# Performance work log

Hardware: AMD Instinct MI355X
Metric: run time of the kernel (lower is better)

Reference implementation:

```python
import jax, jax.numpy as jnp
import numpy as np

N_QUERIES = 32
N_KEYS = 128
INF = 1e10


def setup_inputs() -> dict:
    key = jax.random.key(0)
    kq, kk, kv = jax.random.split(key, 3)
    shape = (1, 16, 16384, 64)  # [B, H, N, d]
    return {
        "q": jax.random.normal(kq, shape, dtype=jnp.float32),
        "k": jax.random.normal(kk, shape, dtype=jnp.float32),
        "v": jax.random.normal(kv, shape, dtype=jnp.float32),
    }


def _local_attention(q, k, v, n_queries=N_QUERIES, n_keys=N_KEYS, inf=INF):
    # Faithful to torch _local_attention -> rearrange_to_dense_trunk -> _attention
    # (note: _attention applies NO 1/sqrt(d) scaling; we match that).
    n, d = q.shape[-2:]
    n_trunks = -(-n // n_queries)
    q_pad = n_trunks * n_queries - n
    pad_left = (n_keys - n_queries) // 2
    pad_right = int((n_trunks - 0.5) * n_queries + n_keys / 2 - n + 0.5)

    batch_dims = q.shape[:-2]
    # q -> [..., T, n_queries, d]
    qp = jnp.pad(q, [(0, 0)] * (q.ndim - 2) + [(0, q_pad), (0, 0)])
    q_t = qp.reshape(*batch_dims, n_trunks, n_queries, d)

    # k/v -> sliding windows [..., T, n_keys, d]; window t covers padded
    # positions [t*n_queries, t*n_queries + n_keys) (== torch unfold).
    win_idx = jnp.arange(n_trunks)[:, None] * n_queries + jnp.arange(n_keys)[None, :]

    def window(x):
        xp = jnp.pad(x, [(0, 0)] * (x.ndim - 2) + [(pad_left, pad_right), (0, 0)])
        return xp[..., win_idx, :]  # [..., T, n_keys, d]

    k_t = window(k)
    v_t = window(v)

    # Mask bias equivalent to the -inf padded attn_bias built in
    # rearrange_to_dense_trunk (attn_bias=None branch).
    t = jnp.arange(n_trunks)[:, None, None]
    qi = jnp.arange(n_queries)[None, :, None]
    kj = jnp.arange(n_keys)[None, None, :]
    key_pos = t * n_queries + kj - pad_left   # global key index
    row_pos = t * n_queries + qi              # global query index
    valid = (key_pos >= 0) & (key_pos < n) & (row_pos < n)
    bias = jnp.where(valid, jnp.zeros((), q.dtype), jnp.asarray(-inf, q.dtype))

    # blocked attention
    w = jnp.einsum('...tqd,...tkd->...tqk', q_t, k_t) + bias
    a = jax.nn.softmax(w, axis=-1)
    o = jnp.einsum('...tqk,...tkd->...tqd', a, v_t)

    o = o.reshape(*batch_dims, n_trunks * n_queries, d)
    return o[..., :n, :]


def reference(q, k, v):
    return _local_attention(q, k, v)
```

## Files before the change

kernel.cpp:

```cpp
#include <hip/hip_runtime.h>
#include <hip/hip_bf16.h>


typedef _Float16 f16x8 __attribute__((ext_vector_type(8)));
typedef _Float16 f16x4 __attribute__((ext_vector_type(4)));
typedef float f32x16 __attribute__((ext_vector_type(16)));
typedef unsigned int u32;
typedef u32 u32x4 __attribute__((ext_vector_type(4)));

#define NSEQ   16384
#define DHEAD  64
#define LOG2E  1.44269504088896340736f
#define TRB    4
#define BQ     (TRB * 32)
#define WROWS  (BQ + 96)
#define RSTR   128
#define KBYTES (WROWS * RSTR)

__device__ __forceinline__ int swz(int r) {
  return ((r & 7) << 4) | ((r & 8) << 3);
}

__device__ __forceinline__ u32 pk2(float a, float b) {
  auto h2 = __builtin_amdgcn_cvt_pkrtz(a, b);
  return __builtin_bit_cast(u32, h2);
}

__device__ __forceinline__ void plswap(u32& a, u32& b) {
#if __has_builtin(__builtin_amdgcn_permlane32_swap)
  typedef u32 u32x2 __attribute__((ext_vector_type(2)));
  u32x2 r = __builtin_amdgcn_permlane32_swap(a, b, false, false);
  a = r[0]; b = r[1];
#else
  const int hi = (threadIdx.x & 63) >> 5;
  u32 sa = (u32)__shfl_xor((int)a, 32);
  u32 sb = (u32)__shfl_xor((int)b, 32);
  u32 na = hi ? sb : a;
  u32 nb = hi ? b : sa;
  a = na; b = nb;
#endif
}

__device__ __forceinline__ void tr8(u32 va, f16x4 (&t)[8]) {
  asm volatile("ds_read_b64_tr_b16 %0, %8 offset:0\n\t"
               "ds_read_b64_tr_b16 %1, %8 offset:1024\n\t"
               "ds_read_b64_tr_b16 %2, %8 offset:512\n\t"
               "ds_read_b64_tr_b16 %3, %8 offset:1536\n\t"
               "ds_read_b64_tr_b16 %4, %8 offset:2048\n\t"
               "ds_read_b64_tr_b16 %5, %8 offset:3072\n\t"
               "ds_read_b64_tr_b16 %6, %8 offset:2560\n\t"
               "ds_read_b64_tr_b16 %7, %8 offset:3584\n\t"
               "s_waitcnt lgkmcnt(0)"
               : "=&v"(t[0]), "=&v"(t[1]), "=&v"(t[2]), "=&v"(t[3]),
                 "=&v"(t[4]), "=&v"(t[5]), "=&v"(t[6]), "=&v"(t[7])
               : "v"(va));
  __builtin_amdgcn_sched_barrier(0);
}

__device__ __forceinline__ int vaddr(int r, int c8) {
  const int dh = c8 >> 4;
  const int idx = ((r >> 2) & 1) * 8 + (dh >> 1) * 4 + ((r >> 3) & 1) * 2 + (dh & 1);
  return (r >> 4) * 2048 + idx * 128 + (r & 3) * 32 + (c8 & 15) * 2;
}

__global__ __launch_bounds__(256, 2) void local_attn_kernel(
    const float* __restrict__ q, const float* __restrict__ k,
    const float* __restrict__ v, float* __restrict__ out) {
  __shared__ __align__(128) char smem[2 * KBYTES];
  char* const Kc = smem;
  char* const Vc = smem + KBYTES;

  const int tid  = threadIdx.x;
  const int wave = tid >> 6;
  const int lane = tid & 63;
  const int l31  = lane & 31;
  const int hi   = lane >> 5;
  const int rsub = tid >> 3;
  const int c8   = (tid & 7) * 8;

  int bid = blockIdx.x;
  bid = (bid & 7) * 256 + (bid >> 3);
  const int h   = bid >> 7;
  const int q0b = (bid & 127) << 7;
  const int kg0 = q0b - 48;
  const int q0  = q0b + wave * 32;
  const int kb0 = q0 - 48;
  const int kvb = wave * 32;

  const float* __restrict__ qh = q + (size_t)h * NSEQ * DHEAD;
  const float* __restrict__ kh = k + (size_t)h * NSEQ * DHEAD;
  const float* __restrict__ vh = v + (size_t)h * NSEQ * DHEAD;

  float4 qr[4][2];
  #pragma unroll
  for (int ks = 0; ks < 4; ++ks) {
    const float* p = qh + (size_t)(q0 + l31) * DHEAD + ks * 16 + hi * 8;
    qr[ks][0] = *reinterpret_cast<const float4*>(p);
    qr[ks][1] = *reinterpret_cast<const float4*>(p + 4);
  }
  float4 kr[7][2], vr[7][2];
  #pragma unroll
  for (int it = 0; it < 7; ++it) {
    const int r = it * 32 + rsub;
    const int g = min(max(kg0 + r, 0), NSEQ - 1);
    const float* pk_ = kh + (size_t)g * DHEAD + c8;
    kr[it][0] = *reinterpret_cast<const float4*>(pk_);
    kr[it][1] = *reinterpret_cast<const float4*>(pk_ + 4);
  }
  #pragma unroll
  for (int it = 0; it < 7; ++it) {
    const int r = it * 32 + rsub;
    const int g = min(max(kg0 + r, 0), NSEQ - 1);
    const float* pv_ = vh + (size_t)g * DHEAD + c8;
    vr[it][0] = *reinterpret_cast<const float4*>(pv_);
    vr[it][1] = *reinterpret_cast<const float4*>(pv_ + 4);
  }
  asm volatile("" ::: "memory");

  #pragma unroll
  for (int it = 0; it < 7; ++it) {
    const int r = it * 32 + rsub;
    const u32x4 w = {pk2(kr[it][0].x, kr[it][0].y), pk2(kr[it][0].z, kr[it][0].w),
                     pk2(kr[it][1].x, kr[it][1].y), pk2(kr[it][1].z, kr[it][1].w)};
    *reinterpret_cast<u32x4*>(Kc + ((r * RSTR + c8 * 2) ^ swz(r))) = w;
  }

  f16x8 qf[4];
  #pragma unroll
  for (int ks = 0; ks < 4; ++ks) {
    qf[ks][0] = (_Float16)(qr[ks][0].x * LOG2E); qf[ks][1] = (_Float16)(qr[ks][0].y * LOG2E);
    qf[ks][2] = (_Float16)(qr[ks][0].z * LOG2E); qf[ks][3] = (_Float16)(qr[ks][0].w * LOG2E);
    qf[ks][4] = (_Float16)(qr[ks][1].x * LOG2E); qf[ks][5] = (_Float16)(qr[ks][1].y * LOG2E);
    qf[ks][6] = (_Float16)(qr[ks][1].z * LOG2E); qf[ks][7] = (_Float16)(qr[ks][1].w * LOG2E);
  }

  __syncthreads();

  f32x16 sacc[4] = {};
  #pragma unroll
  for (int ks = 0; ks < 4; ++ks) {
    #pragma unroll
    for (int kt = 0; kt < 4; ++kt) {
      const int row = kvb + kt * 32 + l31;
      const f16x8 kf = *reinterpret_cast<const f16x8*>(
          Kc + ((row * RSTR + (ks * 16 + hi * 8) * 2) ^ swz(row)));
      sacc[kt] = __builtin_amdgcn_mfma_f32_32x32x16_f16(kf, qf[ks], sacc[kt], 0, 0, 0);
    }
  }

  if (q0 < 48 || q0 > NSEQ - 80) {
    #pragma unroll
    for (int kt = 0; kt < 4; ++kt)
      #pragma unroll
      for (int r = 0; r < 16; ++r) {
        const int key = kb0 + kt * 32 + (r & 3) + 8 * (r >> 2) + 4 * hi;
        if ((unsigned)key >= (unsigned)NSEQ) sacc[kt][r] = -1e30f;
      }
  }

  float mx = -1e30f;
  #pragma unroll
  for (int kt = 0; kt < 4; ++kt)
    #pragma unroll
    for (int r = 0; r < 16; ++r) mx = fmaxf(mx, sacc[kt][r]);
  mx = fmaxf(mx, __shfl_xor(mx, 32));
  float sum = 0.f;
  #pragma unroll
  for (int kt = 0; kt < 4; ++kt)
    #pragma unroll
    for (int r = 0; r < 16; ++r) {
      const float p = exp2f(sacc[kt][r] - mx);
      sacc[kt][r] = p;
      sum += p;
    }
  sum += __shfl_xor(sum, 32);
  const float inv = 1.0f / sum;

  f16x8 pa[4][2];
  #pragma unroll
  for (int kt = 0; kt < 4; ++kt) {
    u32 pk[8];
    #pragma unroll
    for (int c = 0; c < 8; ++c)
      pk[c] = pk2(sacc[kt][2 * c] * inv, sacc[kt][2 * c + 1] * inv);
    plswap(pk[0], pk[2]); plswap(pk[1], pk[3]);
    plswap(pk[4], pk[6]); plswap(pk[5], pk[7]);
    union { f16x8 f; u32 u[4]; } f0, f1;
    f0.u[0] = pk[0]; f0.u[1] = pk[1]; f0.u[2] = pk[2]; f0.u[3] = pk[3];
    f1.u[0] = pk[4]; f1.u[1] = pk[5]; f1.u[2] = pk[6]; f1.u[3] = pk[7];
    pa[kt][0] = f0.f;
    pa[kt][1] = f1.f;
  }

  #pragma unroll
  for (int it = 0; it < 7; ++it) {
    const int r = it * 32 + rsub;
    const u32x4 w = {pk2(vr[it][0].x, vr[it][0].y), pk2(vr[it][0].z, vr[it][0].w),
                     pk2(vr[it][1].x, vr[it][1].y), pk2(vr[it][1].z, vr[it][1].w)};
    *reinterpret_cast<u32x4*>(Vc + vaddr(r, c8)) = w;
  }

  __syncthreads();

  const u32 vb = (u32)(size_t)Vc + (u32)(lane * 8);
  f32x16 oacc[2] = {};
  #pragma unroll
  for (int kt = 0; kt < 4; ++kt) {
    f16x4 t[8];
    tr8(vb + (u32)(2 * (wave + kt) * 2048), t);
    union { f16x8 f; f16x4 h2[2]; } b00, b01, b10, b11;
    b00.h2[0] = t[0]; b00.h2[1] = t[1];
    b01.h2[0] = t[2]; b01.h2[1] = t[3];
    b10.h2[0] = t[4]; b10.h2[1] = t[5];
    b11.h2[0] = t[6]; b11.h2[1] = t[7];
    oacc[0] = __builtin_amdgcn_mfma_f32_32x32x16_f16(pa[kt][0], b00.f, oacc[0], 0, 0, 0);
    oacc[1] = __builtin_amdgcn_mfma_f32_32x32x16_f16(pa[kt][0], b01.f, oacc[1], 0, 0, 0);
    oacc[0] = __builtin_amdgcn_mfma_f32_32x32x16_f16(pa[kt][1], b10.f, oacc[0], 0, 0, 0);
    oacc[1] = __builtin_amdgcn_mfma_f32_32x32x16_f16(pa[kt][1], b11.f, oacc[1], 0, 0, 0);
  }

  float* __restrict__ oh = out + (size_t)h * NSEQ * DHEAD;
  #pragma unroll
  for (int r = 0; r < 16; ++r) {
    const int row = q0 + (r & 3) + 8 * (r >> 2) + 4 * hi;
    float* po = oh + (size_t)row * DHEAD + l31;
    po[0]  = oacc[0][r];
    po[32] = oacc[1][r];
  }
}

extern "C" void kernel_launch(void* const* d_in, const int* in_sizes, int n_in,
                              void* d_out, int out_size, void* d_ws, size_t ws_size,
                              hipStream_t stream) {
  const float* q = (const float*)d_in[0];
  const float* k = (const float*)d_in[1];
  const float* v = (const float*)d_in[2];
  float* out = (float*)d_out;
  dim3 grid(2048), block(256);
  hipLaunchKernelGGL(local_attn_kernel, grid, block, 0, stream, q, k, v, out);
}
```

Baseline: 45.72 us.

## Share one LDS buffer for K and V and raise occupancy to 4 blocks

K and V now share a single LDS buffer. V is loaded from global memory only after the QK^T/softmax phase and a new barrier, instead of being prefetched into registers at kernel start. Dropping the 56 float4 register prefetch and halving shared memory allows launch bounds of 4 blocks per CU for higher occupancy. The cost is that V global-load latency is no longer overlapped with the score computation, plus an extra block-wide barrier.

```diff
diff --git a/kernel.cpp b/kernel.cpp
--- a/kernel.cpp
+++ b/kernel.cpp
@@ -63,12 +63,10 @@
   return (r >> 4) * 2048 + idx * 128 + (r & 3) * 32 + (c8 & 15) * 2;
 }
 
-__global__ __launch_bounds__(256, 2) void local_attn_kernel(
+__global__ __launch_bounds__(256, 4) void local_attn_kernel(
     const float* __restrict__ q, const float* __restrict__ k,
     const float* __restrict__ v, float* __restrict__ out) {
-  __shared__ __align__(128) char smem[2 * KBYTES];
-  char* const Kc = smem;
-  char* const Vc = smem + KBYTES;
+  __shared__ __align__(128) char Bc[KBYTES];
 
   const int tid  = threadIdx.x;
   const int wave = tid >> 6;
@@ -98,31 +96,15 @@
     qr[ks][0] = *reinterpret_cast<const float4*>(p);
     qr[ks][1] = *reinterpret_cast<const float4*>(p + 4);
   }
-  float4 kr[7][2], vr[7][2];
   #pragma unroll
   for (int it = 0; it < 7; ++it) {
     const int r = it * 32 + rsub;
     const int g = min(max(kg0 + r, 0), NSEQ - 1);
     const float* pk_ = kh + (size_t)g * DHEAD + c8;
-    kr[it][0] = *reinterpret_cast<const float4*>(pk_);
-    kr[it][1] = *reinterpret_cast<const float4*>(pk_ + 4);
-  }
-  #pragma unroll
-  for (int it = 0; it < 7; ++it) {
-    const int r = it * 32 + rsub;
-    const int g = min(max(kg0 + r, 0), NSEQ - 1);
-    const float* pv_ = vh + (size_t)g * DHEAD + c8;
-    vr[it][0] = *reinterpret_cast<const float4*>(pv_);
-    vr[it][1] = *reinterpret_cast<const float4*>(pv_ + 4);
-  }
-  asm volatile("" ::: "memory");
-
-  #pragma unroll
-  for (int it = 0; it < 7; ++it) {
-    const int r = it * 32 + rsub;
-    const u32x4 w = {pk2(kr[it][0].x, kr[it][0].y), pk2(kr[it][0].z, kr[it][0].w),
-                     pk2(kr[it][1].x, kr[it][1].y), pk2(kr[it][1].z, kr[it][1].w)};
-    *reinterpret_cast<u32x4*>(Kc + ((r * RSTR + c8 * 2) ^ swz(r))) = w;
+    const float4 a = *reinterpret_cast<const float4*>(pk_);
+    const float4 b = *reinterpret_cast<const float4*>(pk_ + 4);
+    const u32x4 w = {pk2(a.x, a.y), pk2(a.z, a.w), pk2(b.x, b.y), pk2(b.z, b.w)};
+    *reinterpret_cast<u32x4*>(Bc + ((r * RSTR + c8 * 2) ^ swz(r))) = w;
   }
 
   f16x8 qf[4];
@@ -143,7 +125,7 @@
     for (int kt = 0; kt < 4; ++kt) {
       const int row = kvb + kt * 32 + l31;
       const f16x8 kf = *reinterpret_cast<const f16x8*>(
-          Kc + ((row * RSTR + (ks * 16 + hi * 8) * 2) ^ swz(row)));
+          Bc + ((row * RSTR + (ks * 16 + hi * 8) * 2) ^ swz(row)));
       sacc[kt] = __builtin_amdgcn_mfma_f32_32x32x16_f16(kf, qf[ks], sacc[kt], 0, 0, 0);
     }
   }
@@ -192,17 +174,22 @@
     pa[kt][1] = f1.f;
   }
 
+  __syncthreads();
+
   #pragma unroll
   for (int it = 0; it < 7; ++it) {
     const int r = it * 32 + rsub;
-    const u32x4 w = {pk2(vr[it][0].x, vr[it][0].y), pk2(vr[it][0].z, vr[it][0].w),
-                     pk2(vr[it][1].x, vr[it][1].y), pk2(vr[it][1].z, vr[it][1].w)};
-    *reinterpret_cast<u32x4*>(Vc + vaddr(r, c8)) = w;
+    const int g = min(max(kg0 + r, 0), NSEQ - 1);
+    const float* pv_ = vh + (size_t)g * DHEAD + c8;
+    const float4 a = *reinterpret_cast<const float4*>(pv_);
+    const float4 b = *reinterpret_cast<const float4*>(pv_ + 4);
+    const u32x4 w = {pk2(a.x, a.y), pk2(a.z, a.w), pk2(b.x, b.y), pk2(b.z, b.w)};
+    *reinterpret_cast<u32x4*>(Bc + vaddr(r, c8)) = w;
   }
 
   __syncthreads();
 
-  const u32 vb = (u32)(size_t)Vc + (u32)(lane * 8);
+  const u32 vb = (u32)(size_t)(&Bc[0]) + (u32)(lane * 8);
   f32x16 oacc[2] = {};
   #pragma unroll
   for (int kt = 0; kt < 4; ++kt) {
```

New measurement: 48.97 us. 1.07x slower.
